# Kernel tuning notes

Measured on AMD Instinct MI355X. Metric: run time of the kernel, lower is better.

Reference implementation:

```python
import jax, jax.numpy as jnp
import numpy as np

B, D, C = 8192, 128, 64


def setup_inputs() -> dict:
    key = jax.random.key(0)
    k1, k2, k3 = jax.random.split(key, 3)
    embeddings = jax.random.normal(k1, (B, D), dtype=jnp.float32)
    margin_matrix = jax.random.uniform(k2, (C, C), dtype=jnp.float32)
    labels = jax.random.randint(k3, (B,), 0, C, dtype=jnp.int64)
    return {"embeddings": embeddings, "margin_matrix": margin_matrix, "labels": labels}


def reference(embeddings, margin_matrix, labels):
    # Batch-hard mining (indices only, mirrors the detached CPU loop).
    e = jax.lax.stop_gradient(embeddings)
    sq = jnp.sum(e * e, axis=1)                      # [B]
    d2 = sq[:, None] + sq[None, :] - 2.0 * (e @ e.T)  # [B, B] squared dists
    d2 = jnp.maximum(d2, 0.0)

    same = labels[:, None] == labels[None, :]         # [B, B]
    eye = jnp.eye(labels.shape[0], dtype=bool)
    pos_mask = same & ~eye
    neg_mask = ~same

    NEG_INF = jnp.float32(-1e30)
    POS_INF = jnp.float32(1e30)
    hard_pos = jnp.argmax(jnp.where(pos_mask, d2, NEG_INF), axis=1)  # hardest positive
    hard_neg = jnp.argmin(jnp.where(neg_mask, d2, POS_INF), axis=1)  # hardest negative
    valid = pos_mask.any(axis=1) & neg_mask.any(axis=1)

    # Recompute exact distances on differentiable embeddings (as torch.norm does).
    d_ap = jnp.linalg.norm(embeddings - embeddings[hard_pos], axis=1)
    d_an = jnp.linalg.norm(embeddings - embeddings[hard_neg], axis=1)
    margins = margin_matrix[labels, labels[hard_neg]]

    loss = jnp.maximum(d_ap - d_an + margins, 0.0)
    n_valid = jnp.sum(valid.astype(jnp.float32))
    return jnp.sum(jnp.where(valid, loss, 0.0)) / jnp.maximum(n_valid, 1.0)
```

## Files before the change

kernel.cpp:

```cpp
#include <hip/hip_runtime.h>

typedef __attribute__((ext_vector_type(8))) short bf16x8;
typedef __attribute__((ext_vector_type(4))) float f32x4;
typedef unsigned int u32;
typedef unsigned short u16;

#define BB 8192
#define DD 128
#define CC 64
#define NSLICE 16
#define SLICE_COLS 512
#define NTILES 8
#define NBIN 64
#define BINSTRIDE 16

typedef __attribute__((address_space(1))) void gvoid;
typedef __attribute__((address_space(3))) void lvoid;

static __device__ __forceinline__ u16 f2bf(float x) {
    u32 u = __float_as_uint(x);
    return (u16)((u + 0x7FFFu + ((u >> 16) & 1u)) >> 16);
}
static __device__ __forceinline__ u32 umaxu(u32 a, u32 b) { return a > b ? a : b; }
static __device__ __forceinline__ u32 uminu(u32 a, u32 b) { return a < b ? a : b; }

static __device__ __forceinline__ u32 bfi_key(u32 mask, u32 val, u32 idx) {
    u32 r;
    asm("v_bfi_b32 %0, %1, %2, %3" : "=v"(r) : "s"(mask), "v"(val), "v"(idx));
    return r;
}

static __device__ __forceinline__ void gload16(const void* g, void* l) {
    __builtin_amdgcn_global_load_lds((const gvoid*)g, (lvoid*)l, 16, 0, 0);
}

__global__ __launch_bounds__(256) void k_prep(const float* __restrict__ E,
                                              float* __restrict__ sq,
                                              u16* __restrict__ Ebf,
                                              float* __restrict__ bins) {
    if (blockIdx.x == 0 && threadIdx.x < 2 * NBIN)
        bins[(threadIdx.x & (NBIN - 1)) * BINSTRIDE + (threadIdx.x >= NBIN ? NBIN * BINSTRIDE : 0)] = 0.0f;

    int row = blockIdx.x * 4 + (threadIdx.x >> 6);
    int l   = threadIdx.x & 63;
    float2 v = *reinterpret_cast<const float2*>(E + (size_t)row * DD + l * 2);
    ushort2 bv = make_ushort2(f2bf(v.x), f2bf(v.y));
    *reinterpret_cast<ushort2*>(Ebf + (size_t)row * DD + l * 2) = bv;
    float s = v.x * v.x + v.y * v.y;
    #pragma unroll
    for (int m = 32; m; m >>= 1) s += __shfl_xor(s, m);
    if (l == 0) sq[row] = s;
}

__global__ __launch_bounds__(256, 2) void k_mine(const u16* __restrict__ Ebf,
                                                 const float* __restrict__ sq,
                                                 const int* __restrict__ lab,
                                                 u32* __restrict__ pmax,
                                                 u32* __restrict__ pmin) {
    __shared__ uint4 Bt4[3][1024];

    const int tid = threadIdx.x;
    const int l   = tid & 63;
    const int w   = tid >> 6;
    const int l15 = l & 15;
    const int l4  = l >> 4;
    const int rowW = blockIdx.x * 256 + w * 64;
    const int col0 = blockIdx.y * SLICE_COLS;

    bf16x8 a[4][4];
    #pragma unroll
    for (int rb = 0; rb < 4; ++rb)
        #pragma unroll
        for (int kk = 0; kk < 4; ++kk)
            a[rb][kk] = *reinterpret_cast<const bf16x8*>(
                Ebf + (size_t)(rowW + rb * 16 + l15) * DD + kk * 32 + l4 * 8);

    int labr[4][4];
    #pragma unroll
    for (int rb = 0; rb < 4; ++rb)
        #pragma unroll
        for (int e = 0; e < 4; ++e)
            labr[rb][e] = lab[rowW + rb * 16 + l4 * 4 + e];

    u32 kmax[4][4], kmin[4][4];
    #pragma unroll
    for (int rb = 0; rb < 4; ++rb)
        #pragma unroll
        for (int e = 0; e < 4; ++e) { kmax[rb][e] = 0u; kmin[rb][e] = 0xFFFFFFFFu; }

    f32x4 Z = (f32x4){0.f, 0.f, 0.f, 0.f};
    asm volatile("" : "+v"(Z));

    u32 boff[4][4];
    #pragma unroll
    for (int cb = 0; cb < 4; ++cb)
        #pragma unroll
        for (int kk = 0; kk < 4; ++kk) {
            int r = cb * 16 + l15;
            boff[cb][kk] = (u32)(r * 256 + ((kk * 64 + l4 * 16) ^ ((r & 7) << 4)));
        }

    const int srow = tid >> 4;
    const int sx   = (tid & 15) * 16;

    auto stage = [&](int bufi, int tt) {
        const char* gs = (const char*)Ebf + (size_t)(col0 + tt * 64) * 256;
        char* lb = (char*)&Bt4[bufi][0] + w * 1024;
        #pragma unroll
        for (int rd = 0; rd < 4; ++rd) {
            int r = rd * 16 + srow;
            gload16(gs + r * 256 + (sx ^ ((r & 7) << 4)), lb + rd * 4096);
        }
    };

    stage(0, 0);
    const u32 HM = 0xFFFFE000u;
    int cur = 0;

    for (int t = 0; t < NTILES; ++t) {
        int nxt = cur + 1; if (nxt == 3) nxt = 0;
        if (t + 1 < NTILES) {
            stage(nxt, t + 1);
            asm volatile("s_waitcnt vmcnt(4)" ::: "memory");
        } else {
            asm volatile("s_waitcnt vmcnt(0)" ::: "memory");
        }
        __builtin_amdgcn_s_barrier();
        asm volatile("" ::: "memory");

        const char* Bt = (const char*)&Bt4[cur][0];
        const int colT = col0 + t * 64;

        float cbias[4]; int labc[4]; u32 jn[4];
        #pragma unroll
        for (int cb = 0; cb < 4; ++cb) {
            int gj = colT + cb * 16 + l15;
            cbias[cb] = sq[gj] + 1024.0f;
            labc[cb]  = lab[gj];
            jn[cb] = (u32)gj;
        }

        const bool isdiag = (rowW == colT);

        auto tilebody = [&](bool dg) {
            #pragma unroll
            for (int cb = 0; cb < 4; ++cb) {
                bf16x8 b[4];
                #pragma unroll
                for (int kk = 0; kk < 4; ++kk)
                    b[kk] = *reinterpret_cast<const bf16x8*>(Bt + boff[cb][kk]);
                f32x4 acc[4];
                #pragma unroll
                for (int rb = 0; rb < 4; ++rb)
                    acc[rb] = __builtin_amdgcn_mfma_f32_16x16x32_bf16(
                        a[rb][0], b[0], Z, 0, 0, 0);
                #pragma unroll
                for (int kk = 1; kk < 4; ++kk)
                    #pragma unroll
                    for (int rb = 0; rb < 4; ++rb)
                        acc[rb] = __builtin_amdgcn_mfma_f32_16x16x32_bf16(
                            a[rb][kk], b[kk], acc[rb], 0, 0, 0);

                #pragma unroll
                for (int rb = 0; rb < 4; ++rb)
                    #pragma unroll
                    for (int e = 0; e < 4; ++e) {
                        float val = fmaf(acc[rb][e], -2.0f, cbias[cb]);
                        u32 vb = __float_as_uint(val);
                        u32 keyn = bfi_key(HM, vb, jn[cb]);
                        u32 keyx = keyn ^ 0x1FFFu;
                        bool eq = (labr[rb][e] == labc[cb]);
                        bool selfhit = dg && ((rb * 16 + l4 * 4 + e) == (cb * 16 + l15));
                        u32 cx = (eq && !selfhit) ? keyx : 0u;
                        u32 cn = eq ? 0xFFFFFFFFu : keyn;
                        kmax[rb][e] = umaxu(kmax[rb][e], cx);
                        kmin[rb][e] = uminu(kmin[rb][e], cn);
                    }
            }
        };
        if (isdiag) tilebody(true); else tilebody(false);

        cur = nxt;
    }

    #pragma unroll
    for (int rb = 0; rb < 4; ++rb)
        #pragma unroll
        for (int e = 0; e < 4; ++e) {
            u32 kx = kmax[rb][e], kn = kmin[rb][e];
            #pragma unroll
            for (int m = 1; m < 16; m <<= 1) {
                u32 ox = (u32)__shfl_xor((int)kx, m); kx = umaxu(kx, ox);
                u32 on = (u32)__shfl_xor((int)kn, m); kn = uminu(kn, on);
            }
            if (l15 == 0) {
                int row = rowW + rb * 16 + l4 * 4 + e;
                pmax[(size_t)blockIdx.y * BB + row] = kx;
                pmin[(size_t)blockIdx.y * BB + row] = kn;
            }
        }
}

__global__ __launch_bounds__(256) void k_finalize(const float* __restrict__ E,
                                                  const float* __restrict__ M,
                                                  const int* __restrict__ lab,
                                                  const u32* __restrict__ pmax,
                                                  const u32* __restrict__ pmin,
                                                  float* __restrict__ bins) {
    int row = blockIdx.x * 4 + (threadIdx.x >> 6);
    int l   = threadIdx.x & 63;
    int l15 = l & 15;

    u32 kx = pmax[(size_t)l15 * BB + row];
    u32 kn = pmin[(size_t)l15 * BB + row];
    #pragma unroll
    for (int m = 1; m < 16; m <<= 1) {
        u32 ox = (u32)__shfl_xor((int)kx, m); kx = umaxu(kx, ox);
        u32 on = (u32)__shfl_xor((int)kn, m); kn = uminu(kn, on);
    }
    bool valid = (kx != 0u) && (kn != 0xFFFFFFFFu);
    int hp = 8191 - (int)(kx & 0x1FFFu);
    int hn = (int)(kn & 0x1FFFu);

    float2 ei = *reinterpret_cast<const float2*>(E + (size_t)row * DD + l * 2);
    float2 ep = *reinterpret_cast<const float2*>(E + (size_t)hp  * DD + l * 2);
    float2 en = *reinterpret_cast<const float2*>(E + (size_t)hn  * DD + l * 2);
    float dx = ei.x - ep.x, dy = ei.y - ep.y;
    float sap = dx * dx + dy * dy;
    dx = ei.x - en.x; dy = ei.y - en.y;
    float san = dx * dx + dy * dy;
    #pragma unroll
    for (int m = 32; m; m >>= 1) {
        sap += __shfl_xor(sap, m);
        san += __shfl_xor(san, m);
    }
    if (l == 0) {
        float dap = sqrtf(sap), dan = sqrtf(san);
        float mg = M[lab[row] * CC + lab[hn]];
        float lo = fmaxf(dap - dan + mg, 0.0f);
        int bin = row & (NBIN - 1);
        atomicAdd(&bins[bin * BINSTRIDE], valid ? lo : 0.0f);
        atomicAdd(&bins[NBIN * BINSTRIDE + bin * BINSTRIDE], valid ? 1.0f : 0.0f);
    }
}

__global__ __launch_bounds__(64) void k_div(const float* __restrict__ bins,
                                            float* __restrict__ out) {
    int t = threadIdx.x;
    float a = bins[t * BINSTRIDE];
    float b = bins[NBIN * BINSTRIDE + t * BINSTRIDE];
    #pragma unroll
    for (int m = 32; m; m >>= 1) {
        a += __shfl_xor(a, m);
        b += __shfl_xor(b, m);
    }
    if (t == 0) out[0] = a / fmaxf(b, 1.0f);
}

extern "C" void kernel_launch(void* const* d_in, const int* in_sizes, int n_in,
                              void* d_out, int out_size, void* d_ws, size_t ws_size,
                              hipStream_t stream) {
    const float* E   = (const float*)d_in[0];
    const float* M   = (const float*)d_in[1];
    const int*   lab = (const int*)d_in[2];
    float* out = (float*)d_out;

    char* ws = (char*)d_ws;
    u16*   Ebf  = (u16*)ws;        ws += (size_t)BB * DD * 2;
    float* sq   = (float*)ws;      ws += (size_t)BB * 4;
    u32*   pmax = (u32*)ws;        ws += (size_t)NSLICE * BB * 4;
    u32*   pmin = (u32*)ws;        ws += (size_t)NSLICE * BB * 4;
    float* bins = (float*)ws;      ws += (size_t)2 * NBIN * BINSTRIDE * 4;

    k_prep<<<BB / 4, 256, 0, stream>>>(E, sq, Ebf, bins);
    k_mine<<<dim3(BB / 256, NSLICE), 256, 0, stream>>>(Ebf, sq, lab, pmax, pmin);
    k_finalize<<<BB / 4, 256, 0, stream>>>(E, M, lab, pmax, pmin, bins);
    k_div<<<1, 64, 0, stream>>>(bins, out);
}
```

Before: 48.77 us.

## Merge slice partials with global atomics and fold final divide into finalize

Per-slice partial max/min keys are no longer written to a 16x buffer. Instead each mining block does atomicMax/atomicMin into per-row global arrays, which k_prep initializes. The finalize kernel now reads one key per row directly. The last finalize block, found with an atomic counter, performs the final reduction and division, so the separate k_div launch goes away. This trades partial-buffer traffic and a kernel launch for atomic contention and last-block synchronization.

```diff
diff --git a/kernel.cpp b/kernel.cpp
--- a/kernel.cpp
+++ b/kernel.cpp
@@ -13,6 +13,7 @@
 #define NTILES 8
 #define NBIN 64
 #define BINSTRIDE 16
+#define NFBLK (BB / 4)
 
 typedef __attribute__((address_space(1))) void gvoid;
 typedef __attribute__((address_space(3))) void lvoid;
@@ -37,9 +38,21 @@
 __global__ __launch_bounds__(256) void k_prep(const float* __restrict__ E,
                                               float* __restrict__ sq,
                                               u16* __restrict__ Ebf,
-                                              float* __restrict__ bins) {
-    if (blockIdx.x == 0 && threadIdx.x < 2 * NBIN)
-        bins[(threadIdx.x & (NBIN - 1)) * BINSTRIDE + (threadIdx.x >= NBIN ? NBIN * BINSTRIDE : 0)] = 0.0f;
+                                              u32* __restrict__ gmax,
+                                              u32* __restrict__ gmin,
+                                              float* __restrict__ bins,
+                                              u32* __restrict__ cnt) {
+    if (threadIdx.x < 4) {
+        int r = blockIdx.x * 4 + threadIdx.x;
+        gmax[r] = 0u;
+        gmin[r] = 0xFFFFFFFFu;
+    }
+    if (blockIdx.x == 0) {
+        if (threadIdx.x < 2 * NBIN)
+            bins[(threadIdx.x & (NBIN - 1)) * BINSTRIDE +
+                 (threadIdx.x >= NBIN ? NBIN * BINSTRIDE : 0)] = 0.0f;
+        if (threadIdx.x == 0) cnt[0] = 0u;
+    }
 
     int row = blockIdx.x * 4 + (threadIdx.x >> 6);
     int l   = threadIdx.x & 63;
@@ -55,8 +68,8 @@
 __global__ __launch_bounds__(256, 2) void k_mine(const u16* __restrict__ Ebf,
                                                  const float* __restrict__ sq,
                                                  const int* __restrict__ lab,
-                                                 u32* __restrict__ pmax,
-                                                 u32* __restrict__ pmin) {
+                                                 u32* __restrict__ gmax,
+                                                 u32* __restrict__ gmin) {
     __shared__ uint4 Bt4[3][1024];
 
     const int tid = threadIdx.x;
@@ -195,8 +208,8 @@
             }
             if (l15 == 0) {
                 int row = rowW + rb * 16 + l4 * 4 + e;
-                pmax[(size_t)blockIdx.y * BB + row] = kx;
-                pmin[(size_t)blockIdx.y * BB + row] = kn;
+                atomicMax(&gmax[row], kx);
+                atomicMin(&gmin[row], kn);
             }
         }
 }
@@ -204,20 +217,18 @@
 __global__ __launch_bounds__(256) void k_finalize(const float* __restrict__ E,
                                                   const float* __restrict__ M,
                                                   const int* __restrict__ lab,
-                                                  const u32* __restrict__ pmax,
-                                                  const u32* __restrict__ pmin,
-                                                  float* __restrict__ bins) {
+                                                  const u32* __restrict__ gmax,
+                                                  const u32* __restrict__ gmin,
+                                                  float* __restrict__ bins,
+                                                  u32* __restrict__ cnt,
+                                                  float* __restrict__ out) {
+    __shared__ int islast;
+
     int row = blockIdx.x * 4 + (threadIdx.x >> 6);
     int l   = threadIdx.x & 63;
-    int l15 = l & 15;
-
-    u32 kx = pmax[(size_t)l15 * BB + row];
-    u32 kn = pmin[(size_t)l15 * BB + row];
-    #pragma unroll
-    for (int m = 1; m < 16; m <<= 1) {
-        u32 ox = (u32)__shfl_xor((int)kx, m); kx = umaxu(kx, ox);
-        u32 on = (u32)__shfl_xor((int)kn, m); kn = uminu(kn, on);
-    }
+
+    u32 kx = gmax[row];
+    u32 kn = gmin[row];
     bool valid = (kx != 0u) && (kn != 0xFFFFFFFFu);
     int hp = 8191 - (int)(kx & 0x1FFFu);
     int hn = (int)(kn & 0x1FFFu);
@@ -242,19 +253,25 @@
         atomicAdd(&bins[bin * BINSTRIDE], valid ? lo : 0.0f);
         atomicAdd(&bins[NBIN * BINSTRIDE + bin * BINSTRIDE], valid ? 1.0f : 0.0f);
     }
-}
-
-__global__ __launch_bounds__(64) void k_div(const float* __restrict__ bins,
-                                            float* __restrict__ out) {
-    int t = threadIdx.x;
-    float a = bins[t * BINSTRIDE];
-    float b = bins[NBIN * BINSTRIDE + t * BINSTRIDE];
-    #pragma unroll
-    for (int m = 32; m; m >>= 1) {
-        a += __shfl_xor(a, m);
-        b += __shfl_xor(b, m);
-    }
-    if (t == 0) out[0] = a / fmaxf(b, 1.0f);
+
+    asm volatile("s_waitcnt vmcnt(0)" ::: "memory");
+    __syncthreads();
+    if (threadIdx.x == 0) {
+        u32 old = atomicAdd(cnt, 1u);
+        islast = (old == (u32)(NFBLK - 1));
+    }
+    __syncthreads();
+    if (islast && threadIdx.x < 64) {
+        int t = threadIdx.x;
+        float a = atomicAdd(&bins[t * BINSTRIDE], 0.0f);
+        float b = atomicAdd(&bins[NBIN * BINSTRIDE + t * BINSTRIDE], 0.0f);
+        #pragma unroll
+        for (int m = 32; m; m >>= 1) {
+            a += __shfl_xor(a, m);
+            b += __shfl_xor(b, m);
+        }
+        if (t == 0) out[0] = a / fmaxf(b, 1.0f);
+    }
 }
 
 extern "C" void kernel_launch(void* const* d_in, const int* in_sizes, int n_in,
@@ -268,12 +285,12 @@
     char* ws = (char*)d_ws;
     u16*   Ebf  = (u16*)ws;        ws += (size_t)BB * DD * 2;
     float* sq   = (float*)ws;      ws += (size_t)BB * 4;
-    u32*   pmax = (u32*)ws;        ws += (size_t)NSLICE * BB * 4;
-    u32*   pmin = (u32*)ws;        ws += (size_t)NSLICE * BB * 4;
+    u32*   gmax = (u32*)ws;        ws += (size_t)BB * 4;
+    u32*   gmin = (u32*)ws;        ws += (size_t)BB * 4;
     float* bins = (float*)ws;      ws += (size_t)2 * NBIN * BINSTRIDE * 4;
-
-    k_prep<<<BB / 4, 256, 0, stream>>>(E, sq, Ebf, bins);
-    k_mine<<<dim3(BB / 256, NSLICE), 256, 0, stream>>>(Ebf, sq, lab, pmax, pmin);
-    k_finalize<<<BB / 4, 256, 0, stream>>>(E, M, lab, pmax, pmin, bins);
-    k_div<<<1, 64, 0, stream>>>(bins, out);
-}
+    u32*   cnt  = (u32*)ws;        ws += 64;
+
+    k_prep<<<BB / 4, 256, 0, stream>>>(E, sq, Ebf, gmax, gmin, bins, cnt);
+    k_mine<<<dim3(BB / 256, NSLICE), 256, 0, stream>>>(Ebf, sq, lab, gmax, gmin);
+    k_finalize<<<BB / 4, 256, 0, stream>>>(E, M, lab, gmax, gmin, bins, cnt, out);
+}
```

New measurement: 65.94 us. 35.2% more time.
